# Kernel tuning notes

Hardware: AMD Instinct MI355X
Metric: run time of the kernel (lower is better)

The kernel has to match this reference:

```python
import jax, jax.numpy as jnp
import numpy as np

N_SAMPLES = 32768
N_EVENTS = 64
STEP_SIZE = 256  # indices * STEP_SIZE gives the time offset of each event
BATCH = 16


def setup_inputs() -> dict:
    key = jax.random.key(0)
    k1, k2 = jax.random.split(key)
    x = jax.random.normal(k1, (BATCH, N_EVENTS, N_SAMPLES), dtype=jnp.float32)
    # indices in [0, n_samples/step_size] so time + n_samples <= 2*n_samples
    indices = jax.random.randint(k2, (BATCH, N_EVENTS), 0, N_SAMPLES // STEP_SIZE, dtype=jnp.int64)
    return {"x": x, "indices": indices}


def reference(x, indices):
    # x: [B, E, S] event signals; indices: [B, E] int offsets (in units of step_size)
    B, E, S = x.shape
    times = indices * STEP_SIZE  # [B, E]
    # per-sample target positions in the double-length buffer: [B, E, S]
    pos = times[:, :, None].astype(jnp.int32) + jnp.arange(S, dtype=jnp.int32)[None, None, :]

    def scatter_one(vals, p):
        # vals: [E, S], p: [E, S] -> scatter-add into length-2S buffer
        return jnp.zeros(2 * S, vals.dtype).at[p.reshape(-1)].add(vals.reshape(-1))

    out = jax.vmap(scatter_one)(x, pos)  # [B, 2S]
    # truncate to n_samples, add channel dim -> [B, 1, S]
    return out[:, None, :S]
```

## Files before the change

### kernel.cpp

```cpp
#include <hip/hip_runtime.h>

constexpr int B = 16;
constexpr int E = 64;
constexpr int S = 32768;
constexpr int STEP = 256;
constexpr int HALF = 512;
constexpr int GRP  = 16;

__global__ __launch_bounds__(256)
void sparse_audio_gather(const float* __restrict__ x,
                         const int* __restrict__ idx,
                         float* __restrict__ out) {
    const int b     = blockIdx.y;
    const int pr    = blockIdx.x;
    const int lo    = (threadIdx.x < 128);
    const int half  = lo ? pr : (63 - pr);
    const int local = (int)(threadIdx.x & 127);
    const int s0    = half * HALF + local * 4;

    __shared__ int t_lds[E];
    if (threadIdx.x < E) {
        t_lds[threadIdx.x] = idx[b * E + (int)threadIdx.x] * STEP;
    }
    __syncthreads();

    const float* xb = x + (size_t)b * E * S;

    float4 acc = make_float4(0.f, 0.f, 0.f, 0.f);

    for (int e0 = 0; e0 < E; e0 += GRP) {
        float4 v[GRP];
        float  m[GRP];
        #pragma unroll
        for (int j = 0; j < GRP; ++j) {
            const int off  = s0 - t_lds[e0 + j];
            const int offc = off < 0 ? 0 : off;
            m[j] = off < 0 ? 0.0f : 1.0f;
            v[j] = *reinterpret_cast<const float4*>(
                       xb + (size_t)(e0 + j) * S + offc);
        }
        #pragma unroll
        for (int j = 0; j < GRP; ++j) {
            acc.x += m[j] * v[j].x;
            acc.y += m[j] * v[j].y;
            acc.z += m[j] * v[j].z;
            acc.w += m[j] * v[j].w;
        }
    }

    *reinterpret_cast<float4*>(out + (size_t)b * S + s0) = acc;
}

extern "C" void kernel_launch(void* const* d_in, const int* in_sizes, int n_in,
                              void* d_out, int out_size, void* d_ws, size_t ws_size,
                              hipStream_t stream) {
    const float* x   = (const float*)d_in[0];
    const int*   idx = (const int*)d_in[1];
    float*       out = (float*)d_out;

    dim3 grid(S / (2 * HALF), B);
    dim3 block(256);
    sparse_audio_gather<<<grid, block, 0, stream>>>(x, idx, out);
}
```

Before: 176.3 us.

## Sort event offsets in LDS and loop only over active events per wave

Each block ranks the 64 event offsets into a sorted LDS list packed with event ids. Each thread counts how many events start at or before its 256-aligned window and loads only those, in chunks of eight, plus a masked tail chunk. This removes loads and multiply-adds for events that have not started yet. It adds an O(E^2) rank computation, an extra barrier and a per-thread count loop.

```diff
diff --git a/kernel.cpp b/kernel.cpp
--- a/kernel.cpp
+++ b/kernel.cpp
@@ -5,7 +5,7 @@
 constexpr int S = 32768;
 constexpr int STEP = 256;
 constexpr int HALF = 512;
-constexpr int GRP  = 16;
+constexpr int CH = 8;
 
 __global__ __launch_bounds__(256)
 void sparse_audio_gather(const float* __restrict__ x,
@@ -13,38 +13,76 @@
                          float* __restrict__ out) {
     const int b     = blockIdx.y;
     const int pr    = blockIdx.x;
-    const int lo    = (threadIdx.x < 128);
-    const int half  = lo ? pr : (63 - pr);
+    const int half  = (threadIdx.x < 128) ? pr : (63 - pr);
     const int local = (int)(threadIdx.x & 127);
     const int s0    = half * HALF + local * 4;
+    const int wb    = s0 & ~255;
 
-    __shared__ int t_lds[E];
+    __shared__ int t_raw[E];
+    __shared__ int t_sorted[E];
     if (threadIdx.x < E) {
-        t_lds[threadIdx.x] = idx[b * E + (int)threadIdx.x] * STEP;
+        t_raw[threadIdx.x] = idx[b * E + (int)threadIdx.x] * STEP;
+    }
+    __syncthreads();
+    if (threadIdx.x < E) {
+        const int te = t_raw[threadIdx.x];
+        int rank = 0;
+        #pragma unroll
+        for (int j = 0; j < E; ++j) {
+            const int tj = t_raw[j];
+            rank += (tj < te) || (tj == te && j < (int)threadIdx.x);
+        }
+        t_sorted[rank] = (te << 6) | (int)threadIdx.x;
     }
     __syncthreads();
 
+    int nw = 0;
+    #pragma unroll
+    for (int j = 0; j < E; ++j) {
+        nw += ((t_sorted[j] >> 6) <= wb);
+    }
+
     const float* xb = x + (size_t)b * E * S;
-
     float4 acc = make_float4(0.f, 0.f, 0.f, 0.f);
 
-    for (int e0 = 0; e0 < E; e0 += GRP) {
-        float4 v[GRP];
-        float  m[GRP];
+    int j = 0;
+    for (; j + CH <= nw; j += CH) {
+        float4 v[CH];
         #pragma unroll
-        for (int j = 0; j < GRP; ++j) {
-            const int off  = s0 - t_lds[e0 + j];
-            const int offc = off < 0 ? 0 : off;
-            m[j] = off < 0 ? 0.0f : 1.0f;
-            v[j] = *reinterpret_cast<const float4*>(
-                       xb + (size_t)(e0 + j) * S + offc);
+        for (int k = 0; k < CH; ++k) {
+            const int p  = t_sorted[j + k];
+            const int e  = p & 63;
+            const int off = s0 - (p >> 6);
+            v[k] = *reinterpret_cast<const float4*>(xb + (size_t)e * S + off);
         }
         #pragma unroll
-        for (int j = 0; j < GRP; ++j) {
-            acc.x += m[j] * v[j].x;
-            acc.y += m[j] * v[j].y;
-            acc.z += m[j] * v[j].z;
-            acc.w += m[j] * v[j].w;
+        for (int k = 0; k < CH; ++k) {
+            acc.x += v[k].x;
+            acc.y += v[k].y;
+            acc.z += v[k].z;
+            acc.w += v[k].w;
+        }
+    }
+
+    {
+        float4 v[CH];
+        float  m[CH];
+        #pragma unroll
+        for (int k = 0; k < CH; ++k) {
+            const int jj  = (j + k < E) ? (j + k) : (E - 1);
+            const int p   = t_sorted[jj];
+            const int e   = p & 63;
+            const int off = s0 - (p >> 6);
+            const int offc = off < 0 ? 0 : off;
+            m[k] = (j + k < nw) ? 1.0f : 0.0f;
+            v[k] = *reinterpret_cast<const float4*>(xb + (size_t)e * S + offc);
+        }
+        #pragma unroll
+        for (int k = 0; k < CH; ++k) {
+            acc.x += m[k] * v[k].x;
+            acc.y += m[k] * v[k].y;
+            acc.z += m[k] * v[k].z;
+            acc.w += m[k] * v[k].w;
         }
     }
 
```

Measured after the change: 178.5 us. About the same (+1.3%).
